# Optimization experiments

Measured on AMD Instinct MI355X. Metric: run time of the kernel, lower is better.

## Reference

```python
import jax, jax.numpy as jnp
import numpy as np

T = 4          # spiking time steps
TAU = 2.0      # LIF leak
ALPHA = 4.0    # surrogate sigmoid sharpness
EPS = 1e-5     # batchnorm eps
HEADS = 12
SCALE = 0.125

@jax.custom_vjp
def spike(x):
    return (x >= 0).astype(x.dtype)

def _spike_fwd(x):
    return (x >= 0).astype(x.dtype), x

def _spike_bwd(x, g):
    s = jax.nn.sigmoid(ALPHA * x)
    return (g * ALPHA * s * (1.0 - s),)

spike.defvjp(_spike_fwd, _spike_bwd)

def lif(x, threshold):
    # x: (T*B, ...). layer_by_layer LIF: scan membrane over time axis.
    xt = x.reshape((T, -1) + x.shape[1:])
    def step(mem, xi):
        mem = mem + (xi - mem) / TAU
        s = spike(mem - threshold)
        mem = mem * (1.0 - jax.lax.stop_gradient(s))  # hard reset, detached
        return mem, s
    _, spikes = jax.lax.scan(step, jnp.zeros_like(xt[0]), xt)
    return spikes.reshape(x.shape)

def bn(x, gamma, beta):
    # training-mode batchnorm over all axes except channel axis 1
    axes = (0,) + tuple(range(2, x.ndim))
    mean = x.mean(axes, keepdims=True)
    var = x.var(axes, keepdims=True)
    shp = (1, -1) + (1,) * (x.ndim - 2)
    return (x - mean) * jax.lax.rsqrt(var + EPS) * gamma.reshape(shp) + beta.reshape(shp)

def forward(x, q_w, q_gamma, q_beta, k_w, k_gamma, k_beta, v_w, v_gamma, v_beta,
            proj_w, proj_b, proj_gamma, proj_beta,
            fc1_w, fc1_b, bn1_gamma, bn1_beta, fc2_w, fc2_b, bn2_gamma, bn2_beta):
    TB, C, H, W = x.shape
    N = H * W
    dh = C // HEADS
    xf = x.reshape(TB, C, N)

    def qkv_branch(w, g, b):
        y = lif(bn(jnp.einsum('oc,bcn->bon', w, xf), g, b), 1.0)  # (TB,C,N)
        # (TB,C,N) -> (TB,N,C) -> (TB,N,h,d) -> (TB,h,N,d)
        return y.transpose(0, 2, 1).reshape(TB, N, HEADS, dh).transpose(0, 2, 1, 3)

    q = qkv_branch(q_w, q_gamma, q_beta)
    k = qkv_branch(k_w, k_gamma, k_beta)
    v = qkv_branch(v_w, v_gamma, v_beta)

    kv = jnp.einsum('bhnd,bhne->bhde', k, v)          # (TB,h,d,d)
    attn = jnp.einsum('bhnd,bhde->bhne', q, kv) * SCALE  # (TB,h,N,d)
    attn = attn.transpose(0, 1, 3, 2)                 # (TB,h,d,N)
    attn = lif(attn, 0.5).reshape(TB, C, N)

    proj = jnp.einsum('oc,bcn->bon', proj_w, attn) + proj_b[None, :, None]
    proj = lif(bn(proj, proj_gamma, proj_beta), 1.0).reshape(TB, C, H, W)
    x = x + proj

    h1 = jnp.einsum('oc,bchw->bohw', fc1_w, x) + fc1_b.reshape(1, -1, 1, 1)
    h1 = lif(bn(h1, bn1_gamma, bn1_beta), 1.0)
    h2 = jnp.einsum('oc,bchw->bohw', fc2_w, h1) + fc2_b.reshape(1, -1, 1, 1)
    h2 = lif(bn(h2, bn2_gamma, bn2_beta), 1.0)
    return x + h2

def setup_inputs():
    key = jax.random.key(0)
    B, C, H, W = 32, 384, 14, 14
    Hd = 4 * C
    ks = jax.random.split(key, 8)
    sC = 1.0 / np.sqrt(C)
    sH = 1.0 / np.sqrt(Hd)
    return {
        'x': jax.random.normal(ks[0], (T * B, C, H, W), jnp.float32),
        'q_w': jax.random.normal(ks[1], (C, C), jnp.float32) * sC,
        'q_gamma': jnp.ones((C,), jnp.float32), 'q_beta': jnp.zeros((C,), jnp.float32),
        'k_w': jax.random.normal(ks[2], (C, C), jnp.float32) * sC,
        'k_gamma': jnp.ones((C,), jnp.float32), 'k_beta': jnp.zeros((C,), jnp.float32),
        'v_w': jax.random.normal(ks[3], (C, C), jnp.float32) * sC,
        'v_gamma': jnp.ones((C,), jnp.float32), 'v_beta': jnp.zeros((C,), jnp.float32),
        'proj_w': jax.random.normal(ks[4], (C, C), jnp.float32) * sC,
        'proj_b': jnp.zeros((C,), jnp.float32),
        'proj_gamma': jnp.ones((C,), jnp.float32), 'proj_beta': jnp.zeros((C,), jnp.float32),
        'fc1_w': jax.random.normal(ks[5], (Hd, C), jnp.float32) * sC,
        'fc1_b': jnp.zeros((Hd,), jnp.float32),
        'bn1_gamma': jnp.ones((Hd,), jnp.float32), 'bn1_beta': jnp.zeros((Hd,), jnp.float32),
        'fc2_w': jax.random.normal(ks[6], (C, Hd), jnp.float32) * sH,
        'fc2_b': jnp.zeros((C,), jnp.float32),
        'bn2_gamma': jnp.ones((C,), jnp.float32), 'bn2_beta': jnp.zeros((C,), jnp.float32),
    }

def reference(x, q_w, q_gamma, q_beta, k_w, k_gamma, k_beta, v_w, v_gamma, v_beta,
              proj_w, proj_b, proj_gamma, proj_beta,
              fc1_w, fc1_b, bn1_gamma, bn1_beta, fc2_w, fc2_b, bn2_gamma, bn2_beta):
    return forward(x, q_w, q_gamma, q_beta, k_w, k_gamma, k_beta, v_w, v_gamma, v_beta,
                   proj_w, proj_b, proj_gamma, proj_beta,
                   fc1_w, fc1_b, bn1_gamma, bn1_beta, fc2_w, fc2_b, bn2_gamma, bn2_beta)
```

## Files before the change

### kernel.cpp

```cpp
#include <hip/hip_runtime.h>
#include <stdint.h>

#define NBN   25088
#define NTOK  196
#define BATCH 32
#define CDIM  384
#define HDIM  1536
#define NHEAD 12

typedef float f32x4 __attribute__((ext_vector_type(4)));

#define GLDS16(g, l) __builtin_amdgcn_global_load_lds( \
    (const __attribute__((address_space(1))) void*)(g), \
    (__attribute__((address_space(3))) void*)(l), 16, 0, 0)

__global__ __launch_bounds__(256) void k_transpose(const float* __restrict__ x,
                                                   float* __restrict__ xT) {
  int id = blockIdx.x * 256 + threadIdx.x;
  int c = id / NBN;
  int r = id - c * NBN;
  int b = r / NTOK;
  int n = r - b * NTOK;
  xT[id] = x[((size_t)b * CDIM + c) * NTOK + n];
}

__global__ __launch_bounds__(256) void k_wT(const float* __restrict__ src,
                                            float* __restrict__ dst,
                                            int C, int ldd, int coff) {
  __shared__ float t[32][33];
  const int c0 = blockIdx.x * 32, r0 = blockIdx.y * 32;
  const int tx = threadIdx.x & 31, ty = threadIdx.x >> 5;
#pragma unroll
  for (int i = 0; i < 4; ++i)
    t[ty + i * 8][tx] = src[(size_t)(r0 + ty + i * 8) * C + c0 + tx];
  __syncthreads();
#pragma unroll
  for (int i = 0; i < 4; ++i)
    dst[(size_t)(c0 + ty + i * 8) * ldd + coff + r0 + tx] = t[tx][ty + i * 8];
}

template <typename TIN, int MT>
__global__ __launch_bounds__(256, 3) void k_gemm10(
    const float* __restrict__ WT, const TIN* __restrict__ X,
    const float* __restrict__ bias, float* __restrict__ Y,
    double* __restrict__ pS, double* __restrict__ pS2, int K, int Mtot) {
  __shared__ float As[32][MT];
  __shared__ float Bs[32][128];
  constexpr int MR = MT / 16;
  const int tid = threadIdx.x;
  const int lane = tid & 63, wv = tid >> 6;
  const int bn = blockIdx.x, gy = blockIdx.y;
  const int wcol = gy * MT;
  const int tx = tid & 15, ty = tid >> 4;
  const int NK = K >> 5;

  float acc[MR][8];
#pragma unroll
  for (int i = 0; i < MR; ++i)
#pragma unroll
    for (int j = 0; j < 8; ++j) acc[i][j] = 0.f;

  for (int ks = 0; ks < NK; ++ks) {
    const int k0 = ks << 5;
    __syncthreads();
    if constexpr (MT == 128) {
      const int lrow = wv * 2 + (lane >> 5), lcol = (lane & 31) * 4;
#pragma unroll
      for (int i = 0; i < 4; ++i)
        GLDS16(WT + (size_t)(k0 + i * 8 + lrow) * Mtot + wcol + lcol,
               &As[i * 8 + wv * 2][0]);
    } else {
      const int lrow = wv * 4 + (lane >> 4), lcol = (lane & 15) * 4;
#pragma unroll
      for (int i = 0; i < 2; ++i)
        GLDS16(WT + (size_t)(k0 + i * 16 + lrow) * Mtot + wcol + lcol,
               &As[i * 16 + wv * 4][0]);
    }
    if constexpr (__is_same(TIN, float)) {
      const int lrow = wv * 2 + (lane >> 5), lcol = (lane & 31) * 4;
#pragma unroll
      for (int i = 0; i < 4; ++i)
        GLDS16(X + (size_t)(k0 + i * 8 + lrow) * NBN + bn * 128 + lcol,
               &Bs[i * 8 + wv * 2][0]);
    } else {
      const int r = tid >> 3, c16 = tid & 7;
      const uint4 d = *reinterpret_cast<const uint4*>(
          &X[(size_t)(k0 + r) * NBN + bn * 128 + c16 * 16]);
      const uint32_t wd[4] = {d.x, d.y, d.z, d.w};
#pragma unroll
      for (int q = 0; q < 4; ++q) {
        f32x4 f;
        f[0] = (float)(wd[q] & 0xffu);
        f[1] = (float)((wd[q] >> 8) & 0xffu);
        f[2] = (float)((wd[q] >> 16) & 0xffu);
        f[3] = (float)(wd[q] >> 24);
        *reinterpret_cast<f32x4*>(&Bs[r][c16 * 16 + q * 4]) = f;
      }
    }
    asm volatile("s_waitcnt vmcnt(0)" ::: "memory");
    __syncthreads();

    auto lA0 = [&](int kk) { return *reinterpret_cast<const f32x4*>(&As[kk][ty * 4]); };
    auto lA1 = [&](int kk) { return *reinterpret_cast<const f32x4*>(&As[kk][64 + ty * 4]); };
    auto lB0 = [&](int kk) { return *reinterpret_cast<const f32x4*>(&Bs[kk][tx * 4]); };
    auto lB1 = [&](int kk) { return *reinterpret_cast<const f32x4*>(&Bs[kk][64 + tx * 4]); };
    auto FMA = [&](f32x4 a0, f32x4 a1, f32x4 b0, f32x4 b1) {
#pragma unroll
      for (int i = 0; i < MR; ++i) {
        const float av = (i < 4) ? a0[i] : a1[i - 4];
#pragma unroll
        for (int j = 0; j < 8; ++j) {
          const float bv = (j < 4) ? b0[j] : b1[j - 4];
          acc[i][j] = fmaf(av, bv, acc[i][j]);
        }
      }
    };
    f32x4 xa0, xa1, xb0, xb1, ya0, ya1, yb0, yb1;
    xa0 = lA0(0);
    if constexpr (MT == 128) xa1 = lA1(0);
    xb0 = lB0(0);
    xb1 = lB1(0);
#pragma unroll
    for (int kk = 0; kk < 32; kk += 2) {
      ya0 = lA0(kk + 1);
      if constexpr (MT == 128) ya1 = lA1(kk + 1);
      yb0 = lB0(kk + 1);
      yb1 = lB1(kk + 1);
      FMA(xa0, xa1, xb0, xb1);
      if (kk + 2 < 32) {
        xa0 = lA0(kk + 2);
        if constexpr (MT == 128) xa1 = lA1(kk + 2);
        xb0 = lB0(kk + 2);
        xb1 = lB1(kk + 2);
      }
      FMA(ya0, ya1, yb0, yb1);
    }
  }

#pragma unroll
  for (int i = 0; i < MR; ++i) {
    const int rl = (MT == 128) ? ((i < 4) ? (ty * 4 + i) : (64 + ty * 4 + i - 4))
                               : (ty * 4 + i);
    const int row = wcol + rl;
    const float bv = bias ? bias[row] : 0.f;
    float4 o0, o1;
    o0.x = acc[i][0] + bv; o0.y = acc[i][1] + bv;
    o0.z = acc[i][2] + bv; o0.w = acc[i][3] + bv;
    o1.x = acc[i][4] + bv; o1.y = acc[i][5] + bv;
    o1.z = acc[i][6] + bv; o1.w = acc[i][7] + bv;
    *reinterpret_cast<float4*>(&Y[(size_t)row * NBN + bn * 128 + tx * 4]) = o0;
    *reinterpret_cast<float4*>(&Y[(size_t)row * NBN + bn * 128 + 64 + tx * 4]) = o1;
    double s = (double)o0.x + (double)o0.y + (double)o0.z + (double)o0.w +
               (double)o1.x + (double)o1.y + (double)o1.z + (double)o1.w;
    double s2 = (double)o0.x * o0.x + (double)o0.y * o0.y + (double)o0.z * o0.z +
                (double)o0.w * o0.w + (double)o1.x * o1.x + (double)o1.y * o1.y +
                (double)o1.z * o1.z + (double)o1.w * o1.w;
#pragma unroll
    for (int off = 1; off < 16; off <<= 1) {
      s += __shfl_xor(s, off, 64);
      s2 += __shfl_xor(s2, off, 64);
    }
    if (tx == 0) {
      pS[(size_t)bn * Mtot + row] = s;
      pS2[(size_t)bn * Mtot + row] = s2;
    }
  }
}

__global__ __launch_bounds__(64) void k_bn_reduce3(const double* __restrict__ pS,
                                                   const double* __restrict__ pS2,
                                                   float* __restrict__ mean,
                                                   float* __restrict__ rstd, int Mtot) {
  const int ch = blockIdx.x, lane = threadIdx.x;
  double s = 0.0, s2 = 0.0;
  for (int j = lane; j < 196; j += 64) {
    s += pS[(size_t)j * Mtot + ch];
    s2 += pS2[(size_t)j * Mtot + ch];
  }
#pragma unroll
  for (int off = 32; off; off >>= 1) {
    s += __shfl_down(s, off, 64);
    s2 += __shfl_down(s2, off, 64);
  }
  if (lane == 0) {
    double m = s / (double)NBN;
    double v = s2 / (double)NBN - m * m;
    mean[ch] = (float)m;
    rstd[ch] = (float)(1.0 / sqrt(v + 1e-5));
  }
}

__global__ __launch_bounds__(256) void k_lif_pack(const float* __restrict__ Y,
    const float* __restrict__ mean, const float* __restrict__ rstd,
    const float* __restrict__ g0, const float* __restrict__ g1,
    const float* __restrict__ g2, const float* __restrict__ b0,
    const float* __restrict__ b1, const float* __restrict__ b2,
    uint32_t* __restrict__ pk) {
  const int o = blockIdx.x;
  const int b = threadIdx.x >> 3, w = threadIdx.x & 7;
  int br = o / 384, ol = o - br * 384;
  const float g = (br == 0 ? g0 : br == 1 ? g1 : g2)[ol];
  const float be = (br == 0 ? b0 : br == 1 ? b1 : b2)[ol];
  const float m_ = mean[o], rs_ = rstd[o];
  float mem[32];
#pragma unroll
  for (int j = 0; j < 32; ++j) mem[j] = 0.f;
  for (int t = 0; t < 4; ++t) {
    uint32_t word = 0;
    const size_t base = (size_t)o * NBN + (size_t)(t * 32 + b) * NTOK + w * 32;
#pragma unroll
    for (int q = 0; q < 8; ++q) {
      if (w * 32 + q * 4 < NTOK) {
        float4 v4 = *reinterpret_cast<const float4*>(&Y[base + q * 4]);
        float vv[4] = {v4.x, v4.y, v4.z, v4.w};
#pragma unroll
        for (int jj = 0; jj < 4; ++jj) {
          int j = q * 4 + jj;
          float v = ((vv[jj] - m_) * rs_) * g + be;
          float mm = mem[j];
          mm = mm + (v - mm) * 0.5f;
          bool fire = (mm >= 1.0f);
          mem[j] = fire ? 0.f : mm;
          word |= (fire ? 1u : 0u) << j;
        }
      }
    }
    pk[((size_t)o * 128 + t * 32 + b) * 8 + w] = word;
  }
}

__global__ __launch_bounds__(256) void k_lif_u8(const float* __restrict__ Y,
    const float* __restrict__ mean, const float* __restrict__ rstd,
    const float* __restrict__ gamma, const float* __restrict__ beta,
    uint8_t* __restrict__ sp) {
  const int o = blockIdx.x;
  const int b = threadIdx.x >> 3, w = threadIdx.x & 7;
  const float m_ = mean[o], rs_ = rstd[o], g = gamma[o], be = beta[o];
  float mem[32];
#pragma unroll
  for (int j = 0; j < 32; ++j) mem[j] = 0.f;
  for (int t = 0; t < 4; ++t) {
    const size_t base = (size_t)o * NBN + (size_t)(t * 32 + b) * NTOK + w * 32;
    uint32_t words[8];
#pragma unroll
    for (int q = 0; q < 8; ++q) {
      words[q] = 0;
      if (w * 32 + q * 4 < NTOK) {
        float4 v4 = *reinterpret_cast<const float4*>(&Y[base + q * 4]);
        float vv[4] = {v4.x, v4.y, v4.z, v4.w};
#pragma unroll
        for (int jj = 0; jj < 4; ++jj) {
          int j = q * 4 + jj;
          float v = ((vv[jj] - m_) * rs_) * g + be;
          float mm = mem[j];
          mm = mm + (v - mm) * 0.5f;
          bool fire = (mm >= 1.0f);
          mem[j] = fire ? 0.f : mm;
          words[q] |= (fire ? 1u : 0u) << (8 * jj);
        }
      }
    }
    uint32_t* dst = reinterpret_cast<uint32_t*>(const_cast<uint8_t*>(sp) + base);
#pragma unroll
    for (int q = 0; q < 8; ++q)
      if (w * 32 + q * 4 < NTOK) dst[q] = words[q];
  }
}

template <int MODE>
__global__ __launch_bounds__(256) void k_bn_lif(const float* __restrict__ Y,
                                                const float* __restrict__ mean,
                                                const float* __restrict__ rstd,
                                                const float* __restrict__ gamma,
                                                const float* __restrict__ beta,
                                                const float* __restrict__ addsrc,
                                                float* __restrict__ extra) {
  int id = blockIdx.x * 256 + threadIdx.x;
  int o = id / (BATCH * NTOK);
  int r = id - o * (BATCH * NTOK);
  float m_ = mean[o], rs_ = rstd[o], g = gamma[o], be = beta[o];
  float mem = 0.f;
#pragma unroll
  for (int t = 0; t < 4; ++t) {
    size_t idx = (size_t)o * NBN + (size_t)t * (BATCH * NTOK) + r;
    float v = Y[idx];
    v = ((v - m_) * rs_) * g + be;
    mem = mem + (v - mem) * 0.5f;
    bool fire = (mem >= 1.0f);
    float s = fire ? 1.f : 0.f;
    mem = fire ? 0.f : mem;
    if constexpr (MODE == 1) {
      extra[idx] = addsrc[idx] + s;
    } else {
      int b = r / NTOK, n = r - b * NTOK;
      extra[((size_t)(t * BATCH + b) * CDIM + o) * NTOK + n] = addsrc[idx] + s;
    }
  }
}

__global__ __launch_bounds__(256) void k_attn_pop(const uint32_t* __restrict__ pQ,
                                                  const uint32_t* __restrict__ pK,
                                                  const uint32_t* __restrict__ pV,
                                                  uint8_t* __restrict__ spA) {
  __shared__ __align__(16) uint32_t qw[32][8], kw[32][8], vw[32][8];
  __shared__ int kv[32][33];
  __shared__ uint32_t kvb[8][32];
  __shared__ uint32_t qT[NTOK];
  const int bh = blockIdx.x;
  const int b_ = bh / NHEAD, h = bh - b_ * NHEAD;
  const int tid = threadIdx.x;
  const int e = tid >> 3, w = tid & 7;
  float mem[32];
#pragma unroll
  for (int j = 0; j < 32; ++j) mem[j] = 0.f;

  for (int t = 0; t < 4; ++t) {
    const int tb = t * 32 + b_;
    {
      int d = tid >> 3, wo = tid & 7;
      size_t base = ((size_t)(h * 32 + d) * 128 + tb) * 8 + wo;
      qw[d][wo] = pQ[base];
      kw[d][wo] = pK[base];
      vw[d][wo] = pV[base];
    }
    __syncthreads();
    for (int i = tid; i < 1024; i += 256) {
      int d = i >> 5, ee = i & 31;
      const uint64_t* kp = reinterpret_cast<const uint64_t*>(&kw[d][0]);
      const uint64_t* vp = reinterpret_cast<const uint64_t*>(&vw[ee][0]);
      int s = 0;
#pragma unroll
      for (int u = 0; u < 4; ++u) s += __popcll(kp[u] & vp[u]);
      kv[d][ee] = s;
    }
    __syncthreads();
    {
      int bitb = tid >> 5, ee = tid & 31;
      uint32_t mword = 0;
#pragma unroll
      for (int d = 0; d < 32; ++d) mword |= (uint32_t)((kv[d][ee] >> bitb) & 1) << d;
      kvb[bitb][ee] = mword;
    }
    if (tid < NTOK) {
      uint32_t mword = 0;
#pragma unroll
      for (int d = 0; d < 32; ++d)
        mword |= ((qw[d][tid >> 5] >> (tid & 31)) & 1u) << d;
      qT[tid] = mword;
    }
    __syncthreads();
    uint32_t word = 0;
#pragma unroll
    for (int j = 0; j < 32; ++j) {
      int n = w * 32 + j;
      if (n < NTOK) {
        uint32_t qm = qT[n];
        int acc = 0;
#pragma unroll
        for (int bb = 0; bb < 8; ++bb) acc += __popc(qm & kvb[bb][e]) << bb;
        float val = (float)acc * 0.125f;
        float mm = mem[j];
        mm = mm + (val - mm) * 0.5f;
        bool fire = (mm >= 0.5f);
        mem[j] = fire ? 0.f : mm;
        word |= (fire ? 1u : 0u) << j;
      }
    }
    uint8_t* dst = spA + (size_t)(h * 32 + e) * NBN + (size_t)tb * NTOK + w * 32;
#pragma unroll
    for (int q = 0; q < 8; ++q) {
      if (w * 32 + q * 4 < NTOK) {
        uint32_t b4 = ((word >> (q * 4)) & 1u) | (((word >> (q * 4 + 1)) & 1u) << 8) |
                      (((word >> (q * 4 + 2)) & 1u) << 16) |
                      (((word >> (q * 4 + 3)) & 1u) << 24);
        *reinterpret_cast<uint32_t*>(dst + q * 4) = b4;
      }
    }
    __syncthreads();
  }
}

extern "C" void kernel_launch(void* const* d_in, const int* in_sizes, int n_in,
                              void* d_out, int out_size, void* d_ws, size_t ws_size,
                              hipStream_t stream) {
  const float* x          = (const float*)d_in[0];
  const float* q_w        = (const float*)d_in[1];
  const float* q_gamma    = (const float*)d_in[2];
  const float* q_beta     = (const float*)d_in[3];
  const float* k_w        = (const float*)d_in[4];
  const float* k_gamma    = (const float*)d_in[5];
  const float* k_beta     = (const float*)d_in[6];
  const float* v_w        = (const float*)d_in[7];
  const float* v_gamma    = (const float*)d_in[8];
  const float* v_beta     = (const float*)d_in[9];
  const float* proj_w     = (const float*)d_in[10];
  const float* proj_b     = (const float*)d_in[11];
  const float* proj_gamma = (const float*)d_in[12];
  const float* proj_beta  = (const float*)d_in[13];
  const float* fc1_w      = (const float*)d_in[14];
  const float* fc1_b      = (const float*)d_in[15];
  const float* bn1_gamma  = (const float*)d_in[16];
  const float* bn1_beta   = (const float*)d_in[17];
  const float* fc2_w      = (const float*)d_in[18];
  const float* fc2_b      = (const float*)d_in[19];
  const float* bn2_gamma  = (const float*)d_in[20];
  const float* bn2_beta   = (const float*)d_in[21];
  float* out = (float*)d_out;
  char* ws = (char*)d_ws;

  const size_t O_XT   = 0;
  const size_t O_YQ   = 38535168;
  const size_t O_XRES = 154140672;
  const size_t O_PK   = 192675840;
  const size_t O_SPA  = 197394432;
  const size_t O_H1SP = 192675840;
  const size_t O_H1   = 0;
  const size_t O_ST   = 231211008;
  const size_t O_P1   = 154140672;
  const size_t O_P1B  = O_P1 + 1806336;
  const size_t O_QKVT = 197394432;
  const size_t O_PRJT = 192675840;
  const size_t O_P2A  = 192675840;
  const size_t O_P2AB = O_P2A + 2408448;
  const size_t O_F1T  = 197492736;
  const size_t O_P2B  = 0;
  const size_t O_P2BB = 1204224;
  const size_t O_F2T  = 2408448;

  float* xT    = (float*)(ws + O_XT);
  float* yQ    = (float*)(ws + O_YQ);
  float* yB    = (float*)(ws + O_YQ);
  float* h1    = (float*)(ws + O_H1);
  float* xres  = (float*)(ws + O_XRES);
  uint32_t* pkQKV = (uint32_t*)(ws + O_PK);
  uint8_t* spA   = (uint8_t*)(ws + O_SPA);
  uint8_t* h1sp  = (uint8_t*)(ws + O_H1SP);
  float* qkvT  = (float*)(ws + O_QKVT);
  float* projT = (float*)(ws + O_PRJT);
  float* fc1T  = (float*)(ws + O_F1T);
  float* fc2T  = (float*)(ws + O_F2T);
  double* p1S  = (double*)(ws + O_P1);
  double* p1S2 = (double*)(ws + O_P1B);
  double* p2aS  = (double*)(ws + O_P2A);
  double* p2aS2 = (double*)(ws + O_P2AB);
  double* p2bS  = (double*)(ws + O_P2B);
  double* p2bS2 = (double*)(ws + O_P2BB);
  float* mean_ = (float*)(ws + O_ST);
  float* rstd_ = (float*)(ws + O_ST + 6144);

  k_transpose<<<dim3(CDIM * NBN / 256), 256, 0, stream>>>(x, xT);
  k_wT<<<dim3(12, 12), 256, 0, stream>>>(q_w, qkvT, 384, 1152, 0);
  k_wT<<<dim3(12, 12), 256, 0, stream>>>(k_w, qkvT, 384, 1152, 384);
  k_wT<<<dim3(12, 12), 256, 0, stream>>>(v_w, qkvT, 384, 1152, 768);

  k_gemm10<float, 128><<<dim3(196, 9), 256, 0, stream>>>(
      qkvT, xT, (const float*)nullptr, yQ, p1S, p1S2, CDIM, 1152);
  k_bn_reduce3<<<dim3(1152), 64, 0, stream>>>(p1S, p1S2, mean_, rstd_, 1152);
  k_lif_pack<<<dim3(1152), 256, 0, stream>>>(
      yQ, mean_, rstd_, q_gamma, k_gamma, v_gamma, q_beta, k_beta, v_beta, pkQKV);

  k_attn_pop<<<dim3(BATCH * NHEAD), 256, 0, stream>>>(
      pkQKV, pkQKV + 393216, pkQKV + 786432, spA);

  k_wT<<<dim3(12, 12), 256, 0, stream>>>(proj_w, projT, 384, 384, 0);
  k_gemm10<uint8_t, 64><<<dim3(196, 6), 256, 0, stream>>>(
      projT, spA, proj_b, yB, p1S, p1S2, CDIM, 384);
  k_bn_reduce3<<<dim3(384), 64, 0, stream>>>(p1S, p1S2, mean_, rstd_, 384);
  k_bn_lif<1><<<dim3(9408), 256, 0, stream>>>(yB, mean_, rstd_, proj_gamma, proj_beta,
                                              xT, xres);

  k_wT<<<dim3(12, 48), 256, 0, stream>>>(fc1_w, fc1T, 384, 1536, 0);
  k_gemm10<float, 128><<<dim3(196, 12), 256, 0, stream>>>(
      fc1T, xres, fc1_b, h1, p2aS, p2aS2, CDIM, 1536);
  k_bn_reduce3<<<dim3(1536), 64, 0, stream>>>(p2aS, p2aS2, mean_, rstd_, 1536);
  k_lif_u8<<<dim3(1536), 256, 0, stream>>>(h1, mean_, rstd_,
                                           bn1_gamma, bn1_beta, h1sp);

  k_wT<<<dim3(48, 12), 256, 0, stream>>>(fc2_w, fc2T, 1536, 384, 0);
  k_gemm10<uint8_t, 64><<<dim3(196, 6), 256, 0, stream>>>(
      fc2T, h1sp, fc2_b, yB, p2bS, p2bS2, HDIM, 384);
  k_bn_reduce3<<<dim3(384), 64, 0, stream>>>(p2bS, p2bS2, mean_, rstd_, 384);
  k_bn_lif<2><<<dim3(9408), 256, 0, stream>>>(yB, mean_, rstd_, bn2_gamma, bn2_beta,
                                              xres, out);
}
```

Baseline: 1.265 ms.

## Double-buffer GEMM shared-memory tiles to overlap global loads with FMA

Rewrites the fp32 SIMT GEMM as a two-stage software pipeline. The next K-slice of weights and activations is loaded into a second shared-memory buffer, or into registers for the uint8 spike input, while the current slice is computed. Partial vmcnt waits replace the full drain. For float inputs BK drops to 16 so the doubled buffers fit the same LDS budget. The aim is to hide global-load latency behind FMA work, at the cost of a second barrier per iteration and, for fp32 inputs, more loop iterations.

```diff
diff --git a/kernel.cpp b/kernel.cpp
--- a/kernel.cpp
+++ b/kernel.cpp
@@ -40,19 +40,21 @@
 }
 
 template <typename TIN, int MT>
-__global__ __launch_bounds__(256, 3) void k_gemm10(
+__global__ __launch_bounds__(256, 3) void k_gemm11(
     const float* __restrict__ WT, const TIN* __restrict__ X,
     const float* __restrict__ bias, float* __restrict__ Y,
     double* __restrict__ pS, double* __restrict__ pS2, int K, int Mtot) {
-  __shared__ float As[32][MT];
-  __shared__ float Bs[32][128];
+  constexpr bool FB = __is_same(TIN, float);
+  constexpr int BK = FB ? 16 : 32;
   constexpr int MR = MT / 16;
+  __shared__ float As[2][BK][MT];
+  __shared__ float Bs[2][BK][128];
   const int tid = threadIdx.x;
   const int lane = tid & 63, wv = tid >> 6;
   const int bn = blockIdx.x, gy = blockIdx.y;
   const int wcol = gy * MT;
   const int tx = tid & 15, ty = tid >> 4;
-  const int NK = K >> 5;
+  const int NK = K / BK;
 
   float acc[MR][8];
 #pragma unroll
@@ -60,33 +62,43 @@
 #pragma unroll
     for (int j = 0; j < 8; ++j) acc[i][j] = 0.f;
 
-  for (int ks = 0; ks < NK; ++ks) {
-    const int k0 = ks << 5;
-    __syncthreads();
-    if constexpr (MT == 128) {
-      const int lrow = wv * 2 + (lane >> 5), lcol = (lane & 31) * 4;
-#pragma unroll
-      for (int i = 0; i < 4; ++i)
-        GLDS16(WT + (size_t)(k0 + i * 8 + lrow) * Mtot + wcol + lcol,
-               &As[i * 8 + wv * 2][0]);
+  uint4 pendC, pendN;
+
+  auto stageA = [&](int k0, int buf) {
+    if constexpr (FB) {
+      const int lrow = lane >> 5, lcol = (lane & 31) * 4;
+#pragma unroll
+      for (int i = 0; i < 2; ++i)
+        GLDS16(WT + (size_t)(k0 + wv * 4 + i * 2 + lrow) * Mtot + wcol + lcol,
+               &As[buf][wv * 4 + i * 2][0]);
     } else {
-      const int lrow = wv * 4 + (lane >> 4), lcol = (lane & 15) * 4;
+      const int lrow = lane >> 4, lcol = (lane & 15) * 4;
 #pragma unroll
       for (int i = 0; i < 2; ++i)
-        GLDS16(WT + (size_t)(k0 + i * 16 + lrow) * Mtot + wcol + lcol,
-               &As[i * 16 + wv * 4][0]);
-    }
-    if constexpr (__is_same(TIN, float)) {
-      const int lrow = wv * 2 + (lane >> 5), lcol = (lane & 31) * 4;
-#pragma unroll
-      for (int i = 0; i < 4; ++i)
-        GLDS16(X + (size_t)(k0 + i * 8 + lrow) * NBN + bn * 128 + lcol,
-               &Bs[i * 8 + wv * 2][0]);
-    } else {
+        GLDS16(WT + (size_t)(k0 + wv * 8 + i * 4 + lrow) * Mtot + wcol + lcol,
+               &As[buf][wv * 8 + i * 4][0]);
+    }
+  };
+  auto stageBf = [&](int k0, int buf) {
+    if constexpr (FB) {
+      const int lrow = lane >> 5, lcol = (lane & 31) * 4;
+#pragma unroll
+      for (int i = 0; i < 2; ++i)
+        GLDS16(X + (size_t)(k0 + wv * 4 + i * 2 + lrow) * NBN + bn * 128 + lcol,
+               &Bs[buf][wv * 4 + i * 2][0]);
+    }
+  };
+  auto loadBu8 = [&](int k0, uint4& p) {
+    if constexpr (!FB) {
       const int r = tid >> 3, c16 = tid & 7;
-      const uint4 d = *reinterpret_cast<const uint4*>(
+      p = *reinterpret_cast<const uint4*>(
           &X[(size_t)(k0 + r) * NBN + bn * 128 + c16 * 16]);
-      const uint32_t wd[4] = {d.x, d.y, d.z, d.w};
+    }
+  };
+  auto writeBu8 = [&](const uint4& p, int buf) {
+    if constexpr (!FB) {
+      const int r = tid >> 3, c16 = tid & 7;
+      const uint32_t wd[4] = {p.x, p.y, p.z, p.w};
 #pragma unroll
       for (int q = 0; q < 4; ++q) {
         f32x4 f;
@@ -94,47 +106,68 @@
         f[1] = (float)((wd[q] >> 8) & 0xffu);
         f[2] = (float)((wd[q] >> 16) & 0xffu);
         f[3] = (float)(wd[q] >> 24);
-        *reinterpret_cast<f32x4*>(&Bs[r][c16 * 16 + q * 4]) = f;
+        *reinterpret_cast<f32x4*>(&Bs[buf][r][c16 * 16 + q * 4]) = f;
       }
     }
-    asm volatile("s_waitcnt vmcnt(0)" ::: "memory");
+  };
+
+  stageA(0, 0);
+  stageBf(0, 0);
+  loadBu8(0, pendC);
+
+  for (int ks = 0; ks < NK; ++ks) {
+    const int cur = ks & 1, nxt = cur ^ 1;
+    if (ks + 1 < NK) {
+      stageA((ks + 1) * BK, nxt);
+      stageBf((ks + 1) * BK, nxt);
+      loadBu8((ks + 1) * BK, pendN);
+      if constexpr (FB) asm volatile("s_waitcnt vmcnt(4)" ::: "memory");
+      else              asm volatile("s_waitcnt vmcnt(3)" ::: "memory");
+    } else {
+      asm volatile("s_waitcnt vmcnt(0)" ::: "memory");
+    }
+    writeBu8(pendC, cur);
     __syncthreads();
 
-    auto lA0 = [&](int kk) { return *reinterpret_cast<const f32x4*>(&As[kk][ty * 4]); };
-    auto lA1 = [&](int kk) { return *reinterpret_cast<const f32x4*>(&As[kk][64 + ty * 4]); };
-    auto lB0 = [&](int kk) { return *reinterpret_cast<const f32x4*>(&Bs[kk][tx * 4]); };
-    auto lB1 = [&](int kk) { return *reinterpret_cast<const f32x4*>(&Bs[kk][64 + tx * 4]); };
-    auto FMA = [&](f32x4 a0, f32x4 a1, f32x4 b0, f32x4 b1) {
-#pragma unroll
-      for (int i = 0; i < MR; ++i) {
-        const float av = (i < 4) ? a0[i] : a1[i - 4];
-#pragma unroll
-        for (int j = 0; j < 8; ++j) {
-          const float bv = (j < 4) ? b0[j] : b1[j - 4];
-          acc[i][j] = fmaf(av, bv, acc[i][j]);
+    {
+      auto lA0 = [&](int kk) { return *reinterpret_cast<const f32x4*>(&As[cur][kk][ty * 4]); };
+      auto lA1 = [&](int kk) { return *reinterpret_cast<const f32x4*>(&As[cur][kk][64 + ty * 4]); };
+      auto lB0 = [&](int kk) { return *reinterpret_cast<const f32x4*>(&Bs[cur][kk][tx * 4]); };
+      auto lB1 = [&](int kk) { return *reinterpret_cast<const f32x4*>(&Bs[cur][kk][64 + tx * 4]); };
+      auto FMA = [&](f32x4 a0, f32x4 a1, f32x4 b0, f32x4 b1) {
+#pragma unroll
+        for (int i = 0; i < MR; ++i) {
+          const float av = (i < 4) ? a0[i] : a1[i - 4];
+#pragma unroll
+          for (int j = 0; j < 8; ++j) {
+            const float bv = (j < 4) ? b0[j] : b1[j - 4];
+            acc[i][j] = fmaf(av, bv, acc[i][j]);
+          }
         }
+      };
+      f32x4 xa0, xa1, xb0, xb1, ya0, ya1, yb0, yb1;
+      xa0 = lA0(0);
+      if constexpr (MT == 128) xa1 = lA1(0);
+      xb0 = lB0(0);
+      xb1 = lB1(0);
+#pragma unroll
+      for (int kk = 0; kk < BK; kk += 2) {
+        ya0 = lA0(kk + 1);
+        if constexpr (MT == 128) ya1 = lA1(kk + 1);
+        yb0 = lB0(kk + 1);
+        yb1 = lB1(kk + 1);
+        FMA(xa0, xa1, xb0, xb1);
+        if (kk + 2 < BK) {
+          xa0 = lA0(kk + 2);
+          if constexpr (MT == 128) xa1 = lA1(kk + 2);
+          xb0 = lB0(kk + 2);
+          xb1 = lB1(kk + 2);
+        }
+        FMA(ya0, ya1, yb0, yb1);
       }
-    };
-    f32x4 xa0, xa1, xb0, xb1, ya0, ya1, yb0, yb1;
-    xa0 = lA0(0);
-    if constexpr (MT == 128) xa1 = lA1(0);
-    xb0 = lB0(0);
-    xb1 = lB1(0);
-#pragma unroll
-    for (int kk = 0; kk < 32; kk += 2) {
-      ya0 = lA0(kk + 1);
-      if constexpr (MT == 128) ya1 = lA1(kk + 1);
-      yb0 = lB0(kk + 1);
-      yb1 = lB1(kk + 1);
-      FMA(xa0, xa1, xb0, xb1);
-      if (kk + 2 < 32) {
-        xa0 = lA0(kk + 2);
-        if constexpr (MT == 128) xa1 = lA1(kk + 2);
-        xb0 = lB0(kk + 2);
-        xb1 = lB1(kk + 2);
-      }
-      FMA(ya0, ya1, yb0, yb1);
-    }
+    }
+    if constexpr (!FB) pendC = pendN;
+    __syncthreads();
   }
 
 #pragma unroll
@@ -453,7 +486,7 @@
   k_wT<<<dim3(12, 12), 256, 0, stream>>>(k_w, qkvT, 384, 1152, 384);
   k_wT<<<dim3(12, 12), 256, 0, stream>>>(v_w, qkvT, 384, 1152, 768);
 
-  k_gemm10<float, 128><<<dim3(196, 9), 256, 0, stream>>>(
+  k_gemm11<float, 128><<<dim3(196, 9), 256, 0, stream>>>(
       qkvT, xT, (const float*)nullptr, yQ, p1S, p1S2, CDIM, 1152);
   k_bn_reduce3<<<dim3(1152), 64, 0, stream>>>(p1S, p1S2, mean_, rstd_, 1152);
   k_lif_pack<<<dim3(1152), 256, 0, stream>>>(
@@ -463,21 +496,21 @@
       pkQKV, pkQKV + 393216, pkQKV + 786432, spA);
 
   k_wT<<<dim3(12, 12), 256, 0, stream>>>(proj_w, projT, 384, 384, 0);
-  k_gemm10<uint8_t, 64><<<dim3(196, 6), 256, 0, stream>>>(
+  k_gemm11<uint8_t, 64><<<dim3(196, 6), 256, 0, stream>>>(
       projT, spA, proj_b, yB, p1S, p1S2, CDIM, 384);
   k_bn_reduce3<<<dim3(384), 64, 0, stream>>>(p1S, p1S2, mean_, rstd_, 384);
   k_bn_lif<1><<<dim3(9408), 256, 0, stream>>>(yB, mean_, rstd_, proj_gamma, proj_beta,
                                               xT, xres);
 
   k_wT<<<dim3(12, 48), 256, 0, stream>>>(fc1_w, fc1T, 384, 1536, 0);
-  k_gemm10<float, 128><<<dim3(196, 12), 256, 0, stream>>>(
+  k_gemm11<float, 128><<<dim3(196, 12), 256, 0, stream>>>(
       fc1T, xres, fc1_b, h1, p2aS, p2aS2, CDIM, 1536);
   k_bn_reduce3<<<dim3(1536), 64, 0, stream>>>(p2aS, p2aS2, mean_, rstd_, 1536);
   k_lif_u8<<<dim3(1536), 256, 0, stream>>>(h1, mean_, rstd_,
                                            bn1_gamma, bn1_beta, h1sp);
 
   k_wT<<<dim3(48, 12), 256, 0, stream>>>(fc2_w, fc2T, 1536, 384, 0);
-  k_gemm10<uint8_t, 64><<<dim3(196, 6), 256, 0, stream>>>(
+  k_gemm11<uint8_t, 64><<<dim3(196, 6), 256, 0, stream>>>(
       fc2T, h1sp, fc2_b, yB, p2bS, p2bS2, HDIM, 384);
   k_bn_reduce3<<<dim3(384), 64, 0, stream>>>(p2bS, p2bS2, mean_, rstd_, 384);
   k_bn_lif<2><<<dim3(9408), 256, 0, stream>>>(yB, mean_, rstd_, bn2_gamma, bn2_beta,
```

New measurement: 1.333 ms. +5.3%, slower.

## Replace dense fc2 GEMM with bit-packed sparse spike accumulation

Applied to the files above, without the earlier changes.

The dense uint8 fc2 GEMM is replaced by two kernels. The first packs the binary hidden spikes into per-token bitmasks. The second walks the set bits with ctz and sums only the matching rows of the transposed fc2 weight, skipping the zero spikes. BN partial sums are now produced per 4-token block, so the reduce kernel takes a variable partial count (6272 partials instead of 196). Speed depends on spike density; the loop has a data-dependent trip count that diverges across waves, and the final reduction becomes much longer.

```diff
diff --git a/kernel.cpp b/kernel.cpp
--- a/kernel.cpp
+++ b/kernel.cpp
@@ -167,13 +167,78 @@
   }
 }
 
-__global__ __launch_bounds__(64) void k_bn_reduce3(const double* __restrict__ pS,
+__global__ __launch_bounds__(256) void k_repack(const uint8_t* __restrict__ sp,
+                                                uint32_t* __restrict__ bitsT) {
+  __shared__ uint32_t bb[64][48];
+  const int col0 = blockIdx.x * 64;
+  const int c = threadIdx.x & 63, q = threadIdx.x >> 6;
+#pragma unroll
+  for (int wi = 0; wi < 12; ++wi) {
+    const int w = q * 12 + wi;
+    uint32_t word = 0;
+#pragma unroll
+    for (int j = 0; j < 32; ++j)
+      word |= (uint32_t)(sp[(size_t)(32 * w + j) * NBN + col0 + c] & 1) << j;
+    bb[c][w] = word;
+  }
+  __syncthreads();
+  for (int i = threadIdx.x; i < 64 * 48; i += 256)
+    bitsT[(size_t)col0 * 48 + i] = bb[i / 48][i % 48];
+}
+
+__global__ __launch_bounds__(256) void k_spgemm(
+    const uint32_t* __restrict__ bitsT, const float* __restrict__ WT,
+    const float* __restrict__ bias, float* __restrict__ Y,
+    double* __restrict__ pS, double* __restrict__ pS2) {
+  __shared__ float ytile[4][384];
+  const int tid = threadIdx.x;
+  const int lane = tid & 63, wv = tid >> 6;
+  const int c = blockIdx.x * 4 + wv;
+  const uint32_t* wb = bitsT + (size_t)c * 48;
+
+  float a0 = 0.f, a1 = 0.f, a2 = 0.f, a3 = 0.f, a4 = 0.f, a5 = 0.f;
+  for (int w = 0; w < 48; ++w) {
+    uint32_t word = wb[w];
+    while (word) {
+      const int k = w * 32 + __builtin_ctz(word);
+      word &= word - 1;
+      const float* wr = WT + (size_t)k * 384;
+      a0 += wr[lane];
+      a1 += wr[64 + lane];
+      a2 += wr[128 + lane];
+      a3 += wr[192 + lane];
+      a4 += wr[256 + lane];
+      a5 += wr[320 + lane];
+    }
+  }
+  ytile[wv][lane]       = a0 + bias[lane];
+  ytile[wv][64 + lane]  = a1 + bias[64 + lane];
+  ytile[wv][128 + lane] = a2 + bias[128 + lane];
+  ytile[wv][192 + lane] = a3 + bias[192 + lane];
+  ytile[wv][256 + lane] = a4 + bias[256 + lane];
+  ytile[wv][320 + lane] = a5 + bias[320 + lane];
+  __syncthreads();
+  const int c0 = blockIdx.x * 4;
+  for (int r = tid; r < 384; r += 256) {
+    float4 v;
+    v.x = ytile[0][r]; v.y = ytile[1][r]; v.z = ytile[2][r]; v.w = ytile[3][r];
+    *reinterpret_cast<float4*>(&Y[(size_t)r * NBN + c0]) = v;
+    double s = (double)v.x + (double)v.y + (double)v.z + (double)v.w;
+    double s2 = (double)v.x * v.x + (double)v.y * v.y + (double)v.z * v.z +
+                (double)v.w * v.w;
+    pS[(size_t)blockIdx.x * 384 + r] = s;
+    pS2[(size_t)blockIdx.x * 384 + r] = s2;
+  }
+}
+
+__global__ __launch_bounds__(64) void k_bn_reduceN(const double* __restrict__ pS,
                                                    const double* __restrict__ pS2,
                                                    float* __restrict__ mean,
-                                                   float* __restrict__ rstd, int Mtot) {
+                                                   float* __restrict__ rstd,
+                                                   int Mtot, int NP) {
   const int ch = blockIdx.x, lane = threadIdx.x;
   double s = 0.0, s2 = 0.0;
-  for (int j = lane; j < 196; j += 64) {
+  for (int j = lane; j < NP; j += 64) {
     s += pS[(size_t)j * Mtot + ch];
     s2 += pS2[(size_t)j * Mtot + ch];
   }
@@ -423,9 +488,10 @@
   const size_t O_P2A  = 192675840;
   const size_t O_P2AB = O_P2A + 2408448;
   const size_t O_F1T  = 197492736;
-  const size_t O_P2B  = 0;
-  const size_t O_P2BB = 1204224;
-  const size_t O_F2T  = 2408448;
+  const size_t O_BT   = 0;
+  const size_t O_F2T  = 4816896;
+  const size_t O_P2B  = 77070336;
+  const size_t O_P2BB = 96337920;
 
   float* xT    = (float*)(ws + O_XT);
   float* yQ    = (float*)(ws + O_YQ);
@@ -439,6 +505,7 @@
   float* projT = (float*)(ws + O_PRJT);
   float* fc1T  = (float*)(ws + O_F1T);
   float* fc2T  = (float*)(ws + O_F2T);
+  uint32_t* bitsT = (uint32_t*)(ws + O_BT);
   double* p1S  = (double*)(ws + O_P1);
   double* p1S2 = (double*)(ws + O_P1B);
   double* p2aS  = (double*)(ws + O_P2A);
@@ -455,7 +522,7 @@
 
   k_gemm10<float, 128><<<dim3(196, 9), 256, 0, stream>>>(
       qkvT, xT, (const float*)nullptr, yQ, p1S, p1S2, CDIM, 1152);
-  k_bn_reduce3<<<dim3(1152), 64, 0, stream>>>(p1S, p1S2, mean_, rstd_, 1152);
+  k_bn_reduceN<<<dim3(1152), 64, 0, stream>>>(p1S, p1S2, mean_, rstd_, 1152, 196);
   k_lif_pack<<<dim3(1152), 256, 0, stream>>>(
       yQ, mean_, rstd_, q_gamma, k_gamma, v_gamma, q_beta, k_beta, v_beta, pkQKV);
 
@@ -465,21 +532,21 @@
   k_wT<<<dim3(12, 12), 256, 0, stream>>>(proj_w, projT, 384, 384, 0);
   k_gemm10<uint8_t, 64><<<dim3(196, 6), 256, 0, stream>>>(
       projT, spA, proj_b, yB, p1S, p1S2, CDIM, 384);
-  k_bn_reduce3<<<dim3(384), 64, 0, stream>>>(p1S, p1S2, mean_, rstd_, 384);
+  k_bn_reduceN<<<dim3(384), 64, 0, stream>>>(p1S, p1S2, mean_, rstd_, 384, 196);
   k_bn_lif<1><<<dim3(9408), 256, 0, stream>>>(yB, mean_, rstd_, proj_gamma, proj_beta,
                                               xT, xres);
 
   k_wT<<<dim3(12, 48), 256, 0, stream>>>(fc1_w, fc1T, 384, 1536, 0);
   k_gemm10<float, 128><<<dim3(196, 12), 256, 0, stream>>>(
       fc1T, xres, fc1_b, h1, p2aS, p2aS2, CDIM, 1536);
-  k_bn_reduce3<<<dim3(1536), 64, 0, stream>>>(p2aS, p2aS2, mean_, rstd_, 1536);
+  k_bn_reduceN<<<dim3(1536), 64, 0, stream>>>(p2aS, p2aS2, mean_, rstd_, 1536, 196);
   k_lif_u8<<<dim3(1536), 256, 0, stream>>>(h1, mean_, rstd_,
                                            bn1_gamma, bn1_beta, h1sp);
 
   k_wT<<<dim3(48, 12), 256, 0, stream>>>(fc2_w, fc2T, 1536, 384, 0);
-  k_gemm10<uint8_t, 64><<<dim3(196, 6), 256, 0, stream>>>(
-      fc2T, h1sp, fc2_b, yB, p2bS, p2bS2, HDIM, 384);
-  k_bn_reduce3<<<dim3(384), 64, 0, stream>>>(p2bS, p2bS2, mean_, rstd_, 384);
+  k_repack<<<dim3(NBN / 64), 256, 0, stream>>>(h1sp, bitsT);
+  k_spgemm<<<dim3(NBN / 4), 256, 0, stream>>>(bitsT, fc2T, fc2_b, yB, p2bS, p2bS2);
+  k_bn_reduceN<<<dim3(384), 64, 0, stream>>>(p2bS, p2bS2, mean_, rstd_, 384, NBN / 4);
   k_bn_lif<2><<<dim3(9408), 256, 0, stream>>>(yB, mean_, rstd_, bn2_gamma, bn2_beta,
                                               xres, out);
 }
```

After: 1.095 ms. 1.16x faster.
